# Kernel tuning notes

Hardware: AMD Instinct MI355X
Metric: run time of the kernel (lower is better)

The kernel has to match this reference:

```python
import jax, jax.numpy as jnp
import numpy as np
from jax import lax

B, C_IN, H, W = 32, 3, 224, 224
EMBED = 768 // 4  # dim // 4 = 192
K = 3             # kernel_size
STRIDE = 2        # patch_stride
PAD = 1           # patch_padding
BN_EPS = 1e-5


def setup_inputs() -> dict:
    key = jax.random.key(0)
    kx, kw, kb, kg, kbeta = jax.random.split(key, 5)
    x = jax.random.normal(kx, (B, C_IN, H, W), dtype=jnp.float32)
    fan_in = C_IN * K * K
    bound = 1.0 / np.sqrt(fan_in)
    conv_w = jax.random.uniform(kw, (EMBED, C_IN, K, K), jnp.float32, -bound, bound)
    conv_b = jax.random.uniform(kb, (EMBED,), jnp.float32, -bound, bound)
    gamma = jnp.ones((EMBED,), jnp.float32)
    beta = jnp.zeros((EMBED,), jnp.float32)
    return {"x": x, "conv_w": conv_w, "conv_b": conv_b, "gamma": gamma, "beta": beta}


def _patch_embed(x, conv_w, conv_b, gamma, beta):
    # Conv2d(in_chans, embed_dim, k=3, stride=2, pad=1)
    y = lax.conv_general_dilated(
        x, conv_w,
        window_strides=(STRIDE, STRIDE),
        padding=[(PAD, PAD), (PAD, PAD)],
        dimension_numbers=("NCHW", "OIHW", "NCHW"),
    ) + conv_b[None, :, None, None]  # [B, EMBED, 112, 112]
    # BatchNorm2d (training mode: batch statistics, biased variance)
    mean = jnp.mean(y, axis=(0, 2, 3), keepdims=True)
    var = jnp.mean(jnp.square(y - mean), axis=(0, 2, 3), keepdims=True)
    y = (y - mean) * lax.rsqrt(var + BN_EPS)
    y = y * gamma[None, :, None, None] + beta[None, :, None, None]
    # GELU (torch default: exact erf form)
    y = jax.nn.gelu(y, approximate=False)
    # MaxPool2d(kernel=3, stride=2, padding=1)
    y = lax.reduce_window(
        y, -jnp.inf, lax.max,
        window_dimensions=(1, 1, 3, 3),
        window_strides=(1, 1, STRIDE, STRIDE),
        padding=[(0, 0), (0, 0), (PAD, PAD), (PAD, PAD)],
    )  # [B, EMBED, 56, 56]
    return y


def reference(x, conv_w, conv_b, gamma, beta):
    return _patch_embed(x, conv_w, conv_b, gamma, beta)
```

## Files before the change

kernel.cpp:

```cpp
#include <hip/hip_runtime.h>
#include <hip/hip_bf16.h>
#include <math.h>

#define B_   32
#define CIN  3
#define H_   224
#define W_   224
#define OC   192
#define OH   112
#define OW   112
#define PH   56
#define PW   56
#define NSP  (B_*OH*OW)
#define PLANE (OH*OW)
#define CB_STRIDE 68

typedef __attribute__((ext_vector_type(8))) short bf16x8;
typedef __attribute__((ext_vector_type(4))) float f32x4;

static __device__ __forceinline__ unsigned short f2bf(float f) {
    __hip_bfloat16 h = __float2bfloat16(f);
    return *reinterpret_cast<unsigned short*>(&h);
}
static __device__ __forceinline__ float bf_lo(unsigned int u) {
    unsigned int v = u << 16;
    return *reinterpret_cast<float*>(&v);
}
static __device__ __forceinline__ float bf_hi(unsigned int u) {
    unsigned int v = u & 0xffff0000u;
    return *reinterpret_cast<float*>(&v);
}

static __device__ __forceinline__ float fexp2(float x) {
#if __has_builtin(__builtin_amdgcn_exp2f)
    return __builtin_amdgcn_exp2f(x);
#else
    return exp2f(x);
#endif
}
static __device__ __forceinline__ float frcp(float x) {
#if __has_builtin(__builtin_amdgcn_rcpf)
    return __builtin_amdgcn_rcpf(x);
#else
    return 1.0f / x;
#endif
}

static __device__ __forceinline__ float fast_gelu(float x) {
    float x2 = x * x;
    float inner = fmaf(0.044715f * x2, x, x);
    float e = fexp2(inner * 2.3022082f);
    float r = frcp(1.0f + e);
    return x * (e * r);
}

template<int K>
static __device__ __forceinline__ float tapT(const float* __restrict__ xb,
                                             int ihb, int iwb) {
    if constexpr (K == 27) { return 1.0f; }
    else if constexpr (K > 27) { return 0.0f; }
    else {
        constexpr int c = K / 9, r = (K % 9) / 3, j = K % 3;
        int ih = ihb + r, iw = iwb + j;
        bool v = ((unsigned)ih < (unsigned)H_) && ((unsigned)iw < (unsigned)W_);
        return v ? xb[(c * H_ + ih) * W_ + iw] : 0.0f;
    }
}

__global__ void zero_stats(float* stats) {
    if (threadIdx.x < 384) stats[threadIdx.x] = 0.f;
}

__global__ __launch_bounds__(256) void conv_kernel(
    const float* __restrict__ x, const float* __restrict__ w,
    const float* __restrict__ bias, __hip_bfloat16* __restrict__ y,
    float* __restrict__ stats)
{
    __shared__ __align__(16) unsigned int cbuf[OC * CB_STRIDE];
    __shared__ float ssum[2][4 * OC];

    int blk  = blockIdx.x;
    int b    = blk / 98;
    int pb   = (blk - b * 98) * 128;
    int tid  = threadIdx.x;
    int wv   = tid >> 6;
    int lane = tid & 63;
    int lo16 = lane & 15;
    int kg   = lane >> 4;

    bf16x8 Bf[12];
    #pragma unroll
    for (int n = 0; n < 12; ++n) {
        int col = n * 16 + lo16;
        float tw[8];
        if (kg < 3) {
            int base = col * 27 + kg * 8;
            #pragma unroll
            for (int j = 0; j < 8; ++j) tw[j] = w[base + j];
        } else {
            tw[0] = w[col * 27 + 24];
            tw[1] = w[col * 27 + 25];
            tw[2] = w[col * 27 + 26];
            tw[3] = bias[col];
            tw[4] = 0.f; tw[5] = 0.f; tw[6] = 0.f; tw[7] = 0.f;
        }
        #pragma unroll
        for (int j = 0; j < 8; ++j) Bf[n][j] = (short)f2bf(tw[j]);
    }

    const float* xb = x + (size_t)b * CIN * H_ * W_;
    bf16x8 Af[2];
    #pragma unroll
    for (int s = 0; s < 2; ++s) {
        int p  = pb + wv * 32 + s * 16 + lo16;
        int oh = p / OW;
        int ow = p - oh * OW;
        int ihb = 2 * oh - 1, iwb = 2 * ow - 1;
        float tv[8];
        if (kg == 0) {
            tv[0]=tapT<0>(xb,ihb,iwb); tv[1]=tapT<1>(xb,ihb,iwb);
            tv[2]=tapT<2>(xb,ihb,iwb); tv[3]=tapT<3>(xb,ihb,iwb);
            tv[4]=tapT<4>(xb,ihb,iwb); tv[5]=tapT<5>(xb,ihb,iwb);
            tv[6]=tapT<6>(xb,ihb,iwb); tv[7]=tapT<7>(xb,ihb,iwb);
        } else if (kg == 1) {
            tv[0]=tapT<8>(xb,ihb,iwb);  tv[1]=tapT<9>(xb,ihb,iwb);
            tv[2]=tapT<10>(xb,ihb,iwb); tv[3]=tapT<11>(xb,ihb,iwb);
            tv[4]=tapT<12>(xb,ihb,iwb); tv[5]=tapT<13>(xb,ihb,iwb);
            tv[6]=tapT<14>(xb,ihb,iwb); tv[7]=tapT<15>(xb,ihb,iwb);
        } else if (kg == 2) {
            tv[0]=tapT<16>(xb,ihb,iwb); tv[1]=tapT<17>(xb,ihb,iwb);
            tv[2]=tapT<18>(xb,ihb,iwb); tv[3]=tapT<19>(xb,ihb,iwb);
            tv[4]=tapT<20>(xb,ihb,iwb); tv[5]=tapT<21>(xb,ihb,iwb);
            tv[6]=tapT<22>(xb,ihb,iwb); tv[7]=tapT<23>(xb,ihb,iwb);
        } else {
            tv[0]=tapT<24>(xb,ihb,iwb); tv[1]=tapT<25>(xb,ihb,iwb);
            tv[2]=tapT<26>(xb,ihb,iwb); tv[3]=tapT<27>(xb,ihb,iwb);
            tv[4]=tapT<28>(xb,ihb,iwb); tv[5]=tapT<29>(xb,ihb,iwb);
            tv[6]=tapT<30>(xb,ihb,iwb); tv[7]=tapT<31>(xb,ihb,iwb);
        }
        #pragma unroll
        for (int j = 0; j < 8; ++j) Af[s][j] = (short)f2bf(tv[j]);
    }

    f32x4 acc0[12], acc1[12];
    #pragma unroll
    for (int n = 0; n < 12; ++n) {
        acc0[n] = (f32x4){0.f, 0.f, 0.f, 0.f};
        acc1[n] = (f32x4){0.f, 0.f, 0.f, 0.f};
    }
    #pragma unroll
    for (int n = 0; n < 12; ++n) {
        acc0[n] = __builtin_amdgcn_mfma_f32_16x16x32_bf16(Af[0], Bf[n], acc0[n], 0, 0, 0);
        acc1[n] = __builtin_amdgcn_mfma_f32_16x16x32_bf16(Af[1], Bf[n], acc1[n], 0, 0, 0);
    }

    #pragma unroll
    for (int n = 0; n < 12; ++n) {
        float s = 0.f, s2 = 0.f;
        #pragma unroll
        for (int i = 0; i < 4; ++i) {
            float v = acc0[n][i]; s += v; s2 = fmaf(v, v, s2);
            v = acc1[n][i];       s += v; s2 = fmaf(v, v, s2);
        }
        s  += __shfl_xor(s, 16);  s  += __shfl_xor(s, 32);
        s2 += __shfl_xor(s2, 16); s2 += __shfl_xor(s2, 32);
        if (lane < 16) {
            ssum[0][wv * OC + n * 16 + lane] = s;
            ssum[1][wv * OC + n * 16 + lane] = s2;
        }
    }

    #pragma unroll
    for (int n = 0; n < 12; ++n) {
        int oc = n * 16 + lo16;
        int pu = wv * 16 + kg * 2;
        unsigned u01 = (unsigned)f2bf(acc0[n][0]) | ((unsigned)f2bf(acc0[n][1]) << 16);
        unsigned u23 = (unsigned)f2bf(acc0[n][2]) | ((unsigned)f2bf(acc0[n][3]) << 16);
        cbuf[oc * CB_STRIDE + pu]     = u01;
        cbuf[oc * CB_STRIDE + pu + 1] = u23;
        unsigned v01 = (unsigned)f2bf(acc1[n][0]) | ((unsigned)f2bf(acc1[n][1]) << 16);
        unsigned v23 = (unsigned)f2bf(acc1[n][2]) | ((unsigned)f2bf(acc1[n][3]) << 16);
        cbuf[oc * CB_STRIDE + pu + 8] = v01;
        cbuf[oc * CB_STRIDE + pu + 9] = v23;
    }

    __syncthreads();

    unsigned short* yus = reinterpret_cast<unsigned short*>(y);
    int ocr = tid >> 4;
    int ch  = tid & 15;
    #pragma unroll
    for (int ocb = 0; ocb < 12; ++ocb) {
        int oc = ocb * 16 + ocr;
        uint4 v = *reinterpret_cast<uint4*>(&cbuf[oc * CB_STRIDE + ch * 4]);
        *reinterpret_cast<uint4*>(
            yus + (size_t)(b * OC + oc) * PLANE + pb + ch * 8) = v;
    }

    for (int i = tid; i < 2 * OC; i += 256) {
        int which = (i >= OC) ? 1 : 0;
        int oc = i - which * OC;
        float v = ssum[which][oc] + ssum[which][OC + oc] +
                  ssum[which][2 * OC + oc] + ssum[which][3 * OC + oc];
        atomicAdd(&stats[which * OC + oc], v);
    }
}

__global__ __launch_bounds__(256) void pool_kernel(
    const __hip_bfloat16* __restrict__ y, const float* __restrict__ stats,
    const float* __restrict__ gamma, const float* __restrict__ beta,
    float* __restrict__ out)
{
    int g = blockIdx.x * 256 + threadIdx.x;
    int j = g % 7;
    int t = g / 7;
    int ph = t % PH;
    int plane = t / PH;
    int oc = plane % OC;

    const unsigned short* py =
        reinterpret_cast<const unsigned short*>(y) + (size_t)plane * PLANE;

    float cmin[8], cmax[8];
    #pragma unroll
    for (int m = 0; m < 8; ++m) { cmin[m] = INFINITY; cmax[m] = -INFINITY; }

    #pragma unroll
    for (int rr = 0; rr < 3; ++rr) {
        int ih = 2 * ph - 1 + rr;
        if (ih >= 0) {
            const uint4* rp = reinterpret_cast<const uint4*>(py + ih * OW + 16 * j - 8);
            uint4 u0 = rp[0], u1 = rp[1], u2 = rp[2];
            float L[24];
            L[0]=bf_lo(u0.x); L[1]=bf_hi(u0.x); L[2]=bf_lo(u0.y); L[3]=bf_hi(u0.y);
            L[4]=bf_lo(u0.z); L[5]=bf_hi(u0.z); L[6]=bf_lo(u0.w); L[7]=bf_hi(u0.w);
            L[8]=bf_lo(u1.x); L[9]=bf_hi(u1.x); L[10]=bf_lo(u1.y); L[11]=bf_hi(u1.y);
            L[12]=bf_lo(u1.z); L[13]=bf_hi(u1.z); L[14]=bf_lo(u1.w); L[15]=bf_hi(u1.w);
            L[16]=bf_lo(u2.x); L[17]=bf_hi(u2.x); L[18]=bf_lo(u2.y); L[19]=bf_hi(u2.y);
            L[20]=bf_lo(u2.z); L[21]=bf_hi(u2.z); L[22]=bf_lo(u2.w); L[23]=bf_hi(u2.w);

            float l7min = (j == 0) ? INFINITY  : L[7];
            float l7max = (j == 0) ? -INFINITY : L[7];

            cmin[0] = fminf(cmin[0], fminf(fminf(l7min, L[8]), L[9]));
            cmax[0] = fmaxf(cmax[0], fmaxf(fmaxf(l7max, L[8]), L[9]));
            #pragma unroll
            for (int m = 1; m < 8; ++m) {
                cmin[m] = fminf(cmin[m], fminf(fminf(L[7+2*m], L[8+2*m]), L[9+2*m]));
                cmax[m] = fmaxf(cmax[m], fmaxf(fmaxf(L[7+2*m], L[8+2*m]), L[9+2*m]));
            }
        }
    }

    float mean = stats[oc] * (1.0f / (float)NSP);
    float var  = fmaf(-mean, mean, stats[OC + oc] * (1.0f / (float)NSP));
    float inv  = rsqrtf(var + 1e-5f);
    float sc   = gamma[oc] * inv;
    float sh   = fmaf(-mean, sc, beta[oc]);

    float res[8];
    #pragma unroll
    for (int m = 0; m < 8; ++m) {
        float lo = fmaf(cmin[m], sc, sh);
        float hi = fmaf(cmax[m], sc, sh);
        res[m] = fmaxf(fast_gelu(lo), fast_gelu(hi));
    }

    float* ob = out + (size_t)plane * (PH * PW) + ph * PW + 8 * j;
    float4 r0 = {res[0], res[1], res[2], res[3]};
    float4 r1 = {res[4], res[5], res[6], res[7]};
    *reinterpret_cast<float4*>(ob)     = r0;
    *reinterpret_cast<float4*>(ob + 4) = r1;
}

extern "C" void kernel_launch(void* const* d_in, const int* in_sizes, int n_in,
                              void* d_out, int out_size, void* d_ws, size_t ws_size,
                              hipStream_t stream) {
    const float* x     = (const float*)d_in[0];
    const float* w     = (const float*)d_in[1];
    const float* bias  = (const float*)d_in[2];
    const float* gamma = (const float*)d_in[3];
    const float* beta  = (const float*)d_in[4];
    float* out = (float*)d_out;

    float* stats = (float*)d_ws;
    __hip_bfloat16* y = (__hip_bfloat16*)((char*)d_ws + 4096);

    hipLaunchKernelGGL(zero_stats, dim3(1), dim3(384), 0, stream, stats);
    hipLaunchKernelGGL(conv_kernel, dim3(B_ * 98), dim3(256), 0, stream,
                       x, w, bias, y, stats);
    hipLaunchKernelGGL(pool_kernel, dim3(B_ * OC * PH * 7 / 256), dim3(256), 0,
                       stream, y, stats, gamma, beta, out);
}
```

Baseline: 223.6 us.

## Precompute bf16 weight fragments once and halve conv LDS staging buffer

A one-block prep kernel now packs the conv weights and bias into bf16 MFMA B-fragments and zeroes the stats buffer. Each conv block then loads one fragment per MFMA step from global memory, so it no longer repeats the fp32 weight loads and conversions and keeps fewer registers alive. The LDS output staging buffer is halved by writing the channels out in two phases of 96, which lowers LDS use per block and can allow more blocks per CU. The cost is two extra barriers per block and a small additional global read per MFMA.

```diff
diff --git a/kernel.cpp b/kernel.cpp
--- a/kernel.cpp
+++ b/kernel.cpp
@@ -67,16 +67,39 @@
     }
 }
 
-__global__ void zero_stats(float* stats) {
-    if (threadIdx.x < 384) stats[threadIdx.x] = 0.f;
+__global__ void prep_kernel(const float* __restrict__ w,
+                            const float* __restrict__ bias,
+                            float* __restrict__ stats, uint4* __restrict__ bfrag) {
+    int t = threadIdx.x;
+    if (t < 384) stats[t] = 0.f;
+    int n = t >> 6, lane = t & 63;
+    int lo16 = lane & 15, kg = lane >> 4;
+    int col = n * 16 + lo16;
+    float tw[8];
+    if (kg < 3) {
+        int base = col * 27 + kg * 8;
+        #pragma unroll
+        for (int j = 0; j < 8; ++j) tw[j] = w[base + j];
+    } else {
+        tw[0] = w[col * 27 + 24];
+        tw[1] = w[col * 27 + 25];
+        tw[2] = w[col * 27 + 26];
+        tw[3] = bias[col];
+        tw[4] = 0.f; tw[5] = 0.f; tw[6] = 0.f; tw[7] = 0.f;
+    }
+    uint4 u;
+    u.x = (unsigned)f2bf(tw[0]) | ((unsigned)f2bf(tw[1]) << 16);
+    u.y = (unsigned)f2bf(tw[2]) | ((unsigned)f2bf(tw[3]) << 16);
+    u.z = (unsigned)f2bf(tw[4]) | ((unsigned)f2bf(tw[5]) << 16);
+    u.w = (unsigned)f2bf(tw[6]) | ((unsigned)f2bf(tw[7]) << 16);
+    bfrag[t] = u;
 }
 
 __global__ __launch_bounds__(256) void conv_kernel(
-    const float* __restrict__ x, const float* __restrict__ w,
-    const float* __restrict__ bias, __hip_bfloat16* __restrict__ y,
-    float* __restrict__ stats)
+    const float* __restrict__ x, const uint4* __restrict__ bfrag,
+    __hip_bfloat16* __restrict__ y, float* __restrict__ stats)
 {
-    __shared__ __align__(16) unsigned int cbuf[OC * CB_STRIDE];
+    __shared__ __align__(16) unsigned int cbuf[96 * CB_STRIDE];
     __shared__ float ssum[2][4 * OC];
 
     int blk  = blockIdx.x;
@@ -87,26 +110,6 @@
     int lane = tid & 63;
     int lo16 = lane & 15;
     int kg   = lane >> 4;
-
-    bf16x8 Bf[12];
-    #pragma unroll
-    for (int n = 0; n < 12; ++n) {
-        int col = n * 16 + lo16;
-        float tw[8];
-        if (kg < 3) {
-            int base = col * 27 + kg * 8;
-            #pragma unroll
-            for (int j = 0; j < 8; ++j) tw[j] = w[base + j];
-        } else {
-            tw[0] = w[col * 27 + 24];
-            tw[1] = w[col * 27 + 25];
-            tw[2] = w[col * 27 + 26];
-            tw[3] = bias[col];
-            tw[4] = 0.f; tw[5] = 0.f; tw[6] = 0.f; tw[7] = 0.f;
-        }
-        #pragma unroll
-        for (int j = 0; j < 8; ++j) Bf[n][j] = (short)f2bf(tw[j]);
-    }
 
     const float* xb = x + (size_t)b * CIN * H_ * W_;
     bf16x8 Af[2];
@@ -150,8 +153,10 @@
     }
     #pragma unroll
     for (int n = 0; n < 12; ++n) {
-        acc0[n] = __builtin_amdgcn_mfma_f32_16x16x32_bf16(Af[0], Bf[n], acc0[n], 0, 0, 0);
-        acc1[n] = __builtin_amdgcn_mfma_f32_16x16x32_bf16(Af[1], Bf[n], acc1[n], 0, 0, 0);
+        uint4 bu = bfrag[n * 64 + lane];
+        bf16x8 Bf = *reinterpret_cast<bf16x8*>(&bu);
+        acc0[n] = __builtin_amdgcn_mfma_f32_16x16x32_bf16(Af[0], Bf, acc0[n], 0, 0, 0);
+        acc1[n] = __builtin_amdgcn_mfma_f32_16x16x32_bf16(Af[1], Bf, acc1[n], 0, 0, 0);
     }
 
     #pragma unroll
@@ -170,31 +175,35 @@
         }
     }
 
-    #pragma unroll
-    for (int n = 0; n < 12; ++n) {
-        int oc = n * 16 + lo16;
-        int pu = wv * 16 + kg * 2;
-        unsigned u01 = (unsigned)f2bf(acc0[n][0]) | ((unsigned)f2bf(acc0[n][1]) << 16);
-        unsigned u23 = (unsigned)f2bf(acc0[n][2]) | ((unsigned)f2bf(acc0[n][3]) << 16);
-        cbuf[oc * CB_STRIDE + pu]     = u01;
-        cbuf[oc * CB_STRIDE + pu + 1] = u23;
-        unsigned v01 = (unsigned)f2bf(acc1[n][0]) | ((unsigned)f2bf(acc1[n][1]) << 16);
-        unsigned v23 = (unsigned)f2bf(acc1[n][2]) | ((unsigned)f2bf(acc1[n][3]) << 16);
-        cbuf[oc * CB_STRIDE + pu + 8] = v01;
-        cbuf[oc * CB_STRIDE + pu + 9] = v23;
-    }
-
-    __syncthreads();
-
     unsigned short* yus = reinterpret_cast<unsigned short*>(y);
     int ocr = tid >> 4;
     int ch  = tid & 15;
     #pragma unroll
-    for (int ocb = 0; ocb < 12; ++ocb) {
-        int oc = ocb * 16 + ocr;
-        uint4 v = *reinterpret_cast<uint4*>(&cbuf[oc * CB_STRIDE + ch * 4]);
-        *reinterpret_cast<uint4*>(
-            yus + (size_t)(b * OC + oc) * PLANE + pb + ch * 8) = v;
+    for (int ph = 0; ph < 2; ++ph) {
+        __syncthreads();
+        #pragma unroll
+        for (int nn = 0; nn < 6; ++nn) {
+            int n   = ph * 6 + nn;
+            int ocl = nn * 16 + lo16;
+            int pu  = wv * 16 + kg * 2;
+            unsigned u01 = (unsigned)f2bf(acc0[n][0]) | ((unsigned)f2bf(acc0[n][1]) << 16);
+            unsigned u23 = (unsigned)f2bf(acc0[n][2]) | ((unsigned)f2bf(acc0[n][3]) << 16);
+            cbuf[ocl * CB_STRIDE + pu]     = u01;
+            cbuf[ocl * CB_STRIDE + pu + 1] = u23;
+            unsigned v01 = (unsigned)f2bf(acc1[n][0]) | ((unsigned)f2bf(acc1[n][1]) << 16);
+            unsigned v23 = (unsigned)f2bf(acc1[n][2]) | ((unsigned)f2bf(acc1[n][3]) << 16);
+            cbuf[ocl * CB_STRIDE + pu + 8] = v01;
+            cbuf[ocl * CB_STRIDE + pu + 9] = v23;
+        }
+        __syncthreads();
+        #pragma unroll
+        for (int ocb = 0; ocb < 6; ++ocb) {
+            int ocl = ocb * 16 + ocr;
+            int oc  = ph * 96 + ocl;
+            uint4 v = *reinterpret_cast<uint4*>(&cbuf[ocl * CB_STRIDE + ch * 4]);
+            *reinterpret_cast<uint4*>(
+                yus + (size_t)(b * OC + oc) * PLANE + pb + ch * 8) = v;
+        }
     }
 
     for (int i = tid; i < 2 * OC; i += 256) {
@@ -284,11 +293,13 @@
     float* out = (float*)d_out;
 
     float* stats = (float*)d_ws;
-    __hip_bfloat16* y = (__hip_bfloat16*)((char*)d_ws + 4096);
-
-    hipLaunchKernelGGL(zero_stats, dim3(1), dim3(384), 0, stream, stats);
+    uint4* bfrag = (uint4*)((char*)d_ws + 2048);
+    __hip_bfloat16* y = (__hip_bfloat16*)((char*)d_ws + 16384);
+
+    hipLaunchKernelGGL(prep_kernel, dim3(1), dim3(768), 0, stream,
+                       w, bias, stats, bfrag);
     hipLaunchKernelGGL(conv_kernel, dim3(B_ * 98), dim3(256), 0, stream,
-                       x, w, bias, y, stats);
+                       x, bfrag, y, stats);
     hipLaunchKernelGGL(pool_kernel, dim3(B_ * OC * PH * 7 / 256), dim3(256), 0,
                        stream, y, stats, gamma, beta, out);
 }
```

New measurement: 222.7 us. No clear change (-0.4%).
